# Performance work log

Hardware: AMD Instinct MI355X
Metric: run time of the kernel (lower is better)

The kernel has to match this reference:

```python
import jax, jax.numpy as jnp
import numpy as np
from jax import lax

B, T, S, J, D = 8, 512, 32, 64, 400
R, MDU, TAGS = 256, 100, 7


def _lstm(x, Wih, Whh, bih, bhh):
    """PyTorch-convention LSTM over x [N,L,Din]; gate order i,f,g,o.
    Returns (hs, cs) each [N,L,R] in scan order (not re-flipped)."""
    N = x.shape[0]
    Rh = Whh.shape[1]
    h0 = jnp.zeros((N, Rh), x.dtype)
    xW = x @ Wih.T + (bih + bhh)  # precompute input projection [N,L,4R]

    def step(carry, xt):
        h, c = carry
        g = xt + h @ Whh.T
        i, f, gg, o = jnp.split(g, 4, axis=-1)
        c = jax.nn.sigmoid(f) * c + jax.nn.sigmoid(i) * jnp.tanh(gg)
        h = jax.nn.sigmoid(o) * jnp.tanh(c)
        return (h, c), (h, c)

    _, (hs, cs) = lax.scan(step, (h0, h0), xW.transpose(1, 0, 2))
    return hs.transpose(1, 0, 2), cs.transpose(1, 0, 2)


def setup_inputs() -> dict:
    key = jax.random.key(0)
    ks = jax.random.split(key, 40)

    def rn(i, shape, s=0.1):
        return s * jax.random.normal(ks[i], shape, jnp.float32)

    inp = {
        'input_text': rn(0, (B, T, D), 1.0),
        'input_syn': rn(1, (B, S, J, D), 1.0),
        'label': jax.random.randint(ks[2], (B, T), 0, TAGS),
        'len_context': jnp.full((B,), T, jnp.int32),
        'len_synopsis': jnp.full((B, S), J, jnp.int32),
    }
    # 6 LSTM parameter sets: context f1/b1 (in=D), synopsis f/b (in=D), modeling f/b (in=4R)
    idx = 3
    for name, din in [('f1', D), ('b1', D), ('sf', D), ('sb', D), ('mf', 4 * R), ('mb', 4 * R)]:
        inp['Wih_' + name] = rn(idx, (4 * R, din)); idx += 1
        inp['Whh_' + name] = rn(idx, (4 * R, R)); idx += 1
        inp['bih_' + name] = rn(idx, (4 * R,)); idx += 1
        inp['bhh_' + name] = rn(idx, (4 * R,)); idx += 1
    inp['W_cWh'] = rn(idx, (MDU, 2 * R)); idx += 1
    inp['W_cWu'] = rn(idx, (MDU, 2 * R)); idx += 1
    inp['W_v'] = rn(idx, (1, MDU)); idx += 1
    inp['W_sWh'] = rn(idx, (2 * R, 2 * R)); idx += 1
    inp['W_sWu'] = rn(idx, (2 * R, 2 * R)); idx += 1
    inp['W_Ws'] = rn(idx, (MDU, 2 * R)); idx += 1
    inp['W_out'] = rn(idx, (TAGS, 6 * R)); idx += 1
    inp['b_out'] = rn(idx, (TAGS,)); idx += 1
    return inp


def reference(input_text, input_syn, label, len_context, len_synopsis,
              Wih_f1, Whh_f1, bih_f1, bhh_f1,
              Wih_b1, Whh_b1, bih_b1, bhh_b1,
              Wih_sf, Whh_sf, bih_sf, bhh_sf,
              Wih_sb, Whh_sb, bih_sb, bhh_sb,
              Wih_mf, Whh_mf, bih_mf, bhh_mf,
              Wih_mb, Whh_mb, bih_mb, bhh_mb,
              W_cWh, W_cWu, W_v, W_sWh, W_sWu, W_Ws, W_out, b_out):
    B_, T_, D_ = input_text.shape
    S_, J_ = input_syn.shape[1], input_syn.shape[2]

    mask = (jnp.arange(T_)[None, :] < len_context[:, None]).astype(input_text.dtype)

    # --- representation layer: manual bi-LSTMCell; backward hiddens kept in scan order ---
    hs_f, cs_f = _lstm(input_text, Wih_f1, Whh_f1, bih_f1, bhh_f1)
    hs_b, cs_b = _lstm(input_text[:, ::-1], Wih_b1, Whh_b1, bih_b1, bhh_b1)
    H = jnp.concatenate([hs_f, hs_b], -1) * mask[..., None]   # [B,T,2R]
    m = jnp.concatenate([cs_f, cs_b], -1) * mask[..., None]   # [B,T,2R]
    x_init = jnp.zeros((B_, 1, 2 * R), input_text.dtype)
    H_full = jnp.concatenate([x_init, H], 1)                  # H_ : [B,T+1,2R]

    # --- synopsis encoder: bi-LSTM final hidden per synopsis sentence ---
    syn = input_syn.reshape(B_ * S_, J_, D_)
    sh_f, _ = _lstm(syn, Wih_sf, Whh_sf, bih_sf, bhh_sf)
    sh_b, _ = _lstm(syn[:, ::-1], Wih_sb, Whh_sb, bih_sb, bhh_sb)
    U = jnp.concatenate([sh_f[:, -1], sh_b[:, -1]], -1).reshape(B_, S_, 2 * R)

    # --- 'ff' co-attention ---
    cWh = H @ W_cWh.T                                          # [B,T,MDU]
    cWu = U @ W_cWu.T                                          # [B,S,MDU]
    z = jnp.tanh(cWh[:, :, None, :] + cWu[:, None, :, :]) @ W_v[0]  # [B,T,S]
    alpha = jax.nn.softmax(z, axis=-1)
    c = jnp.einsum('bts,bsd->btd', alpha, U)                   # [B,T,2R]

    # --- sentinel (ATT_SYN) ---
    Hprev = H_full[:, :T_]                                     # shifted: x_init, H[0..T-2]
    e = jax.nn.sigmoid(Hprev @ W_sWh.T + Hprev @ W_sWu.T)
    s = e * jnp.tanh(m)                                        # [B,T,2R]
    z_hat = jnp.tanh(s @ W_Ws.T + cWh) @ W_v[0]                # [B,T]
    alpha_hat = jax.nn.softmax(jnp.concatenate([z, z_hat[..., None]], -1), axis=-1)
    beta = alpha_hat[:, :, S_:S_ + 1]                          # [B,T,1]
    c_hat = beta * s + (1.0 - beta) * c
    G = jnp.concatenate([H, c_hat], -1)                        # [B,T,4R]

    # --- modeling bi-LSTM (standard aligned outputs) + output projection ---
    mh_f, _ = _lstm(G, Wih_mf, Whh_mf, bih_mf, bhh_mf)
    mh_b, _ = _lstm(G[:, ::-1], Wih_mb, Whh_mb, bih_mb, bhh_mb)
    M = jnp.concatenate([mh_f, mh_b[:, ::-1]], -1)             # [B,T,2R]

    logit = jnp.concatenate([G, M], -1) @ W_out.T + b_out      # [B,T,TAGS]
    return logit
```

## Files before the change

### kernel.cpp

```cpp
#include <hip/hip_runtime.h>
#include <math.h>
#include <stddef.h>


#define BB 8
#define TT 512
#define SS 32
#define JJ 64
#define DD 400
#define RR 256
#define G4 1024
#define H2 512
#define MDU_ 100
#define TAGS_ 7
#define BT (BB*TT)
#define NSEQ (BB*SS)
#define SCH 64
#define MB1 (1024*1024)

typedef __attribute__((ext_vector_type(8))) short short8;
typedef __attribute__((ext_vector_type(4))) float floatx4;
typedef __attribute__((ext_vector_type(4))) unsigned int u32x4;
typedef unsigned short u16;
typedef unsigned int u32;

__device__ __forceinline__ float us2f(u16 u) {
    unsigned int v = ((unsigned int)u) << 16;
    return __builtin_bit_cast(float, v);
}
__device__ __forceinline__ u16 f2us(float f) {
    unsigned int v = __builtin_bit_cast(unsigned int, f);
    v += 0x7FFFu + ((v >> 16) & 1u);
    return (u16)(v >> 16);
}
__device__ __forceinline__ float ldin(const void* p, long i, int bf) {
    return bf ? us2f(((const u16*)p)[i]) : ((const float*)p)[i];
}
__device__ __forceinline__ float sigm(float x) { return 1.0f / (1.0f + expf(-x)); }
__device__ __forceinline__ float sigm_f(float x) { return 1.0f / (1.0f + __expf(-x)); }
__device__ __forceinline__ float tanh_f(float x) {
    float e = __expf(-2.0f * fabsf(x));
    float t = (1.0f - e) / (1.0f + e);
    return copysignf(t, x);
}

__global__ void detect_k(const void* x, int* flag) {
    __shared__ int cnt;
    if (threadIdx.x == 0) cnt = 0;
    __syncthreads();
    u16 lo = ((const u16*)x)[threadIdx.x * 2];
    int e = (lo >> 7) & 0xFF;
    if (e >= 118 && e <= 131) atomicAdd(&cnt, 1);
    __syncthreads();
    if (threadIdx.x == 0) *flag = (cnt > 128) ? 1 : 0;
}
__global__ void castbf_k(const void* src, long off, u16* dst, long n, const int* flag) {
    long i = (long)blockIdx.x * 256 + threadIdx.x;
    if (i < n) dst[i] = (*flag) ? ((const u16*)src)[off + i] : f2us(((const float*)src)[off + i]);
}
__global__ void castf_k(const void* src, float* dst, long n, const int* flag) {
    long i = (long)blockIdx.x * 256 + threadIdx.x;
    if (i < n) dst[i] = ldin(src, i, *flag);
}
__global__ void zero_k(u32* p, long n) {
    long i = (long)blockIdx.x * 256 + threadIdx.x;
    if (i < n) p[i] = 0u;
}
__global__ void bias_sum_k(const void* bih, const void* bhh, float* out, const int* flag) {
    int i = blockIdx.x * 256 + threadIdx.x;
    if (i < G4) out[i] = ldin(bih, i, *flag) + ldin(bhh, i, *flag);
}
__global__ void wsum_k(const void* a, const void* b, u16* o, const int* flag) {
    int i = blockIdx.x * 256 + threadIdx.x;
    if (i < H2 * H2) o[i] = f2us(ldin(a, i, *flag) + ldin(b, i, *flag));
}
__global__ void whh_frag_k(const void* Whh, u16* WF, const int* flag) {
    int i = blockIdx.x * 256 + threadIdx.x;
    if (i >= 4 * 4 * 4 * 8 * 64 * 8) return;
    int j  = i & 7;
    int ln = (i >> 3) & 63;
    int c  = (i >> 9) & 7;
    int t  = (i >> 12) & 3;
    int w  = (i >> 14) & 3;
    int s  = (i >> 16) & 3;
    int n_g = w * 256 + s * 64 + t * 16 + (ln & 15);
    int k   = c * 32 + (ln >> 4) * 8 + j;
    WF[i] = f2us(ldin(Whh, (long)n_g * 256 + k, *flag));
}

#define BM 128
#define BN 128
#define BK 32
#define LDT 40

__global__ __launch_bounds__(256)
void gemm_bt(const u16* __restrict__ A, int lda,
             const u16* __restrict__ W, int ldw,
             void* __restrict__ C, int ldc,
             const float* __restrict__ bias,
             int M, int N, int K, int outBf16)
{
    __shared__ alignas(16) short As[BM * LDT];
    __shared__ alignas(16) short Bs[BN * LDT];
    const int tid  = threadIdx.x;
    const int m0   = blockIdx.y * BM;
    const int n0   = blockIdx.x * BN;
    const int lane = tid & 63;
    const int wave = tid >> 6;
    const int wm   = wave >> 1, wn = wave & 1;
    const int quad = lane >> 4, mrow = lane & 15;

    floatx4 acc[4][4];
#pragma unroll
    for (int i = 0; i < 4; ++i)
#pragma unroll
        for (int j = 0; j < 4; ++j) { floatx4 z4 = {0.f,0.f,0.f,0.f}; acc[i][j] = z4; }

    for (int k0 = 0; k0 < K; k0 += BK) {
#pragma unroll
        for (int cc = 0; cc < 2; ++cc) {
            int c   = tid + cc * 256;
            int row = c >> 2;
            int kc  = (c & 3) << 3;
            int gk  = k0 + kc;
            {
                int gr = m0 + row;
                short8 v;
                if (gr < M && gk + 8 <= K) {
                    v = *(const short8*)(A + (size_t)gr * lda + gk);
                } else {
#pragma unroll
                    for (int e = 0; e < 8; ++e)
                        v[e] = (gr < M && (gk + e) < K) ? (short)A[(size_t)gr * lda + gk + e] : (short)0;
                }
                *(short8*)&As[row * LDT + kc] = v;
            }
            {
                int gn = n0 + row;
                short8 v;
                if (gn < N && gk + 8 <= K) {
                    v = *(const short8*)(W + (size_t)gn * ldw + gk);
                } else {
#pragma unroll
                    for (int e = 0; e < 8; ++e)
                        v[e] = (gn < N && (gk + e) < K) ? (short)W[(size_t)gn * ldw + gk + e] : (short)0;
                }
                *(short8*)&Bs[row * LDT + kc] = v;
            }
        }
        __syncthreads();

        short8 af[4], bf[4];
#pragma unroll
        for (int i = 0; i < 4; ++i)
            af[i] = *(const short8*)&As[(wm * 64 + i * 16 + mrow) * LDT + quad * 8];
#pragma unroll
        for (int j = 0; j < 4; ++j)
            bf[j] = *(const short8*)&Bs[(wn * 64 + j * 16 + mrow) * LDT + quad * 8];
#pragma unroll
        for (int i = 0; i < 4; ++i)
#pragma unroll
            for (int j = 0; j < 4; ++j)
                acc[i][j] = __builtin_amdgcn_mfma_f32_16x16x32_bf16(af[i], bf[j], acc[i][j], 0, 0, 0);
        __syncthreads();
    }

#pragma unroll
    for (int i = 0; i < 4; ++i)
#pragma unroll
        for (int j = 0; j < 4; ++j)
#pragma unroll
            for (int r = 0; r < 4; ++r) {
                int row = m0 + wm * 64 + i * 16 + quad * 4 + r;
                int col = n0 + wn * 64 + j * 16 + mrow;
                if (row < M && col < N) {
                    float v = acc[i][j][r];
                    if (bias) v += bias[col];
                    if (outBf16) ((u16*)C)[(size_t)row * ldc + col] = f2us(v);
                    else         ((float*)C)[(size_t)row * ldc + col] = v;
                }
            }
}

__global__ __launch_bounds__(256, 1)
void lstm_coop(const u16* __restrict__ xWf, const u16* __restrict__ xWb,
               const u16* __restrict__ WFf, const u16* __restrict__ WFb,
               int L,
               u16* __restrict__ hOut, int hStride,
               u16* __restrict__ cOut, int cStride,
               const int* __restrict__ lenp,
               int writeAtSource, int lastOnly, int seqBase,
               u32* __restrict__ hx32, u32* __restrict__ flags,
               int grpBase, int nb, int G8)
{
    const int wgid = blockIdx.x;
    const int s    = wgid / G8;
    const int g    = wgid - s * G8;
    if (g >= 2 * nb) return;
    const int dir  = g / nb;
    const int bat  = g - dir * nb;
    const int tid = threadIdx.x;
    const int wv  = tid >> 6;
    const int ln  = tid & 63;
    const int q   = ln >> 4, m = ln & 15;
    const u16* xW = dir ? xWb : xWf;
    const u16* WF = dir ? WFb : WFf;
    const int grp = grpBase + g;
    u32* flg = flags + (size_t)grp * 64;
    u32* hx  = hx32 + (size_t)grp * 2048;

    __shared__ float g_s[4 * 8 * 64];

    short8 bw[4][8];
    {
        const u16* wb = WF + ((size_t)(s * 4 + wv) * 32) * 512 + ln * 8;
#pragma unroll
        for (int t4 = 0; t4 < 4; ++t4)
#pragma unroll
            for (int c = 0; c < 8; ++c)
                bw[t4][c] = *(const short8*)(wb + (size_t)(t4 * 8 + c) * 512);
    }

    const int seqU = tid >> 5;
    const int j0   = (tid & 31) * 2;
    const int gcol = s * 64 + j0;
    const int mylen = lenp ? lenp[bat * 8 + seqU] : 0x7fffffff;
    float cR0 = 0.f, cR1 = 0.f;

    u32 px0, px1, px2, px3;
    {
        const int tt0 = dir ? (L - 1) : 0;
        const u16* xr = xW + (((size_t)(bat * 8 + seqU)) * L + tt0) * G4 + gcol;
        px0 = *(const u32*)xr;
        px1 = *(const u32*)(xr + 256);
        px2 = *(const u32*)(xr + 512);
        px3 = *(const u32*)(xr + 768);
    }

    for (int t = 0; t < L; ++t) {
        const int tt = dir ? (L - 1 - t) : t;
        short8 a[8];
        if (t > 0) {
            const u32* hp = hx + ((t - 1) & 1) * 1024 + m * 128;
#pragma unroll
            for (int c = 0; c < 8; ++c) {
                if (m < 8) {
                    u32x4 v = *(const u32x4*)(hp + c * 16 + q * 4);
                    a[c] = __builtin_bit_cast(short8, v);
                } else {
                    short8 z = {0,0,0,0,0,0,0,0}; a[c] = z;
                }
            }
        } else {
            short8 z = {0,0,0,0,0,0,0,0};
#pragma unroll
            for (int c = 0; c < 8; ++c) a[c] = z;
        }
        floatx4 acc[4];
#pragma unroll
        for (int t4 = 0; t4 < 4; ++t4) { floatx4 z4 = {0.f,0.f,0.f,0.f}; acc[t4] = z4; }
#pragma unroll
        for (int c = 0; c < 8; ++c)
#pragma unroll
            for (int t4 = 0; t4 < 4; ++t4)
                acc[t4] = __builtin_amdgcn_mfma_f32_16x16x32_bf16(a[c], bw[t4][c], acc[t4], 0, 0, 0);
        if (q < 2) {
#pragma unroll
            for (int t4 = 0; t4 < 4; ++t4)
#pragma unroll
                for (int r = 0; r < 4; ++r)
                    g_s[(wv * 8 + q * 4 + r) * 64 + t4 * 16 + m] = acc[t4][r];
        }
        __syncthreads();
        float hn0, hn1, cn0, cn1;
        {
            float i0 = g_s[(0 * 8 + seqU) * 64 + j0]     + us2f((u16)(px0 & 0xffffu));
            float i1 = g_s[(0 * 8 + seqU) * 64 + j0 + 1] + us2f((u16)(px0 >> 16));
            float f0 = g_s[(1 * 8 + seqU) * 64 + j0]     + us2f((u16)(px1 & 0xffffu));
            float f1 = g_s[(1 * 8 + seqU) * 64 + j0 + 1] + us2f((u16)(px1 >> 16));
            float g0 = g_s[(2 * 8 + seqU) * 64 + j0]     + us2f((u16)(px2 & 0xffffu));
            float g1 = g_s[(2 * 8 + seqU) * 64 + j0 + 1] + us2f((u16)(px2 >> 16));
            float o0 = g_s[(3 * 8 + seqU) * 64 + j0]     + us2f((u16)(px3 & 0xffffu));
            float o1 = g_s[(3 * 8 + seqU) * 64 + j0 + 1] + us2f((u16)(px3 >> 16));
            cn0 = sigm_f(f0) * cR0 + sigm_f(i0) * tanh_f(g0);
            cn1 = sigm_f(f1) * cR1 + sigm_f(i1) * tanh_f(g1);
            hn0 = sigm_f(o0) * tanh_f(cn0);
            hn1 = sigm_f(o1) * tanh_f(cn1);
            cR0 = cn0;
            cR1 = cn1;
            u32 hpack = (u32)f2us(hn0) | ((u32)f2us(hn1) << 16);
            __hip_atomic_store(hx + (t & 1) * 1024 + seqU * 128 + (gcol >> 1),
                               hpack, __ATOMIC_RELAXED, __HIP_MEMORY_SCOPE_AGENT);
        }
        asm volatile("s_waitcnt vmcnt(0)" ::: "memory");
        __syncthreads();
        const bool last = (t == L - 1);
        if (tid == 0 && !last)
            __hip_atomic_store(&flg[s * 16], (u32)(t + 1),
                               __ATOMIC_RELEASE, __HIP_MEMORY_SCOPE_AGENT);
        if (!lastOnly) {
            int wr = writeAtSource ? tt : t;
            float mk = (wr >= mylen) ? 0.f : 1.f;
            size_t ro = ((size_t)(bat * 8 + seqU)) * L + wr;
            u32 hp2 = (u32)f2us(hn0 * mk) | ((u32)f2us(hn1 * mk) << 16);
            *(u32*)(hOut + ro * hStride + dir * RR + gcol) = hp2;
            if (cOut) {
                u32 cp2 = (u32)f2us(cn0 * mk) | ((u32)f2us(cn1 * mk) << 16);
                *(u32*)(cOut + ro * cStride + dir * RR + gcol) = cp2;
            }
        } else if (last) {
            size_t ro = (size_t)(seqBase + bat * 8 + seqU);
            u32 hp2 = (u32)f2us(hn0) | ((u32)f2us(hn1) << 16);
            *(u32*)(hOut + ro * hStride + dir * RR + gcol) = hp2;
        }
        if (!last) {
            {
                const int tn = dir ? (L - 2 - t) : (t + 1);
                const u16* xr = xW + (((size_t)(bat * 8 + seqU)) * L + tn) * G4 + gcol;
                px0 = *(const u32*)xr;
                px1 = *(const u32*)(xr + 256);
                px2 = *(const u32*)(xr + 512);
                px3 = *(const u32*)(xr + 768);
            }
            if (tid == 0) {
                const u32 tgt = (u32)(t + 1);
                long guard = 0;
                for (;;) {
                    u32 f0 = __hip_atomic_load(&flg[0],  __ATOMIC_RELAXED, __HIP_MEMORY_SCOPE_AGENT);
                    u32 f1 = __hip_atomic_load(&flg[16], __ATOMIC_RELAXED, __HIP_MEMORY_SCOPE_AGENT);
                    u32 f2 = __hip_atomic_load(&flg[32], __ATOMIC_RELAXED, __HIP_MEMORY_SCOPE_AGENT);
                    u32 f3 = __hip_atomic_load(&flg[48], __ATOMIC_RELAXED, __HIP_MEMORY_SCOPE_AGENT);
                    if (f0 >= tgt && f1 >= tgt && f2 >= tgt && f3 >= tgt) break;
                    if (++guard > (1L << 18)) break;
                    if (guard > 32) __builtin_amdgcn_s_sleep(1);
                }
                __builtin_amdgcn_fence(__ATOMIC_ACQUIRE, "agent");
            }
            __syncthreads();
        }
    }
}

__global__ void hprev_k(const u16* __restrict__ G, u16* __restrict__ Hp) {
    int idx = blockIdx.x * 256 + threadIdx.x;
    if (idx < BT * H2) {
        int r = idx >> 9, d = idx & 511;
        int t = r & (TT - 1);
        Hp[idx] = (t == 0) ? (u16)0 : G[(size_t)(r - 1) * G4 + d];
    }
}
__global__ void s_k(const float* __restrict__ e, const u16* __restrict__ mB,
                    u16* __restrict__ sB) {
    int i = blockIdx.x * 256 + threadIdx.x;
    if (i < BT * H2) sB[i] = f2us(sigm(e[i]) * tanhf(us2f(mB[i])));
}
__global__ void z_k(const float* __restrict__ cWh, const float* __restrict__ cWu,
                    const float* __restrict__ Wv, float* __restrict__ z) {
    int idx = blockIdx.x * 256 + threadIdx.x;
    if (idx >= BT * SS) return;
    int r = idx >> 5, s = idx & 31;
    int b = r >> 9;
    const float* ph = cWh + (size_t)r * MDU_;
    const float* pu = cWu + (size_t)(b * SS + s) * MDU_;
    float acc = 0.f;
    for (int j = 0; j < MDU_; ++j) acc += tanhf(ph[j] + pu[j]) * Wv[j];
    z[idx] = acc;
}
__global__ void zhat_k(const float* __restrict__ sW, const float* __restrict__ cWh,
                       const float* __restrict__ Wv, float* __restrict__ zhat) {
    int r = blockIdx.x * 256 + threadIdx.x;
    if (r >= BT) return;
    float acc = 0.f;
    const float* ps = sW + (size_t)r * MDU_;
    const float* ph = cWh + (size_t)r * MDU_;
    for (int j = 0; j < MDU_; ++j) acc += tanhf(ps[j] + ph[j]) * Wv[j];
    zhat[r] = acc;
}
__global__ __launch_bounds__(64)
void attn_mix_k(const float* __restrict__ z, const float* __restrict__ zhat,
                const u16* __restrict__ U, const u16* __restrict__ sB,
                u16* __restrict__ G) {
    int r = blockIdx.x;
    int lane = threadIdx.x;
    int b = r >> 9;
    __shared__ float alpha[SS];
    float zv = (lane < SS) ? z[(size_t)r * SS + lane] : -1e30f;
    float mx = zv;
    for (int o = 32; o > 0; o >>= 1) mx = fmaxf(mx, __shfl_xor(mx, o));
    float ez = (lane < SS) ? expf(zv - mx) : 0.f;
    float s1 = ez;
    for (int o = 32; o > 0; o >>= 1) s1 += __shfl_xor(s1, o);
    float zh = zhat[r];
    float mx2 = fmaxf(mx, zh);
    float denom = s1 * expf(mx - mx2) + expf(zh - mx2);
    float beta = expf(zh - mx2) / denom;
    if (lane < SS) alpha[lane] = ez / s1;
    __syncthreads();
    for (int d = lane; d < H2; d += 64) {
        float cv = 0.f;
#pragma unroll 8
        for (int s2 = 0; s2 < SS; ++s2)
            cv += alpha[s2] * us2f(U[(size_t)(b * SS + s2) * H2 + d]);
        float sv = us2f(sB[(size_t)r * H2 + d]);
        G[(size_t)r * G4 + H2 + d] = f2us(beta * sv + (1.f - beta) * cv);
    }
}
__global__ __launch_bounds__(256)
void logit_k(const u16* __restrict__ G, const u16* __restrict__ Mb,
             const u16* __restrict__ Wout, const float* __restrict__ boutF,
             void* __restrict__ out, const int* __restrict__ flag) {
    int r = blockIdx.x * 4 + (threadIdx.x >> 6);
    if (r >= BT) return;
    int lane = threadIdx.x & 63;
    float acc[TAGS_] = {0, 0, 0, 0, 0, 0, 0};
    for (int k = lane; k < 1536; k += 64) {
        float v = (k < G4) ? us2f(G[(size_t)r * G4 + k]) : us2f(Mb[(size_t)r * H2 + (k - G4)]);
#pragma unroll
        for (int tg = 0; tg < TAGS_; ++tg) acc[tg] += v * us2f(Wout[tg * 1536 + k]);
    }
#pragma unroll
    for (int tg = 0; tg < TAGS_; ++tg) {
        float s = acc[tg];
        for (int o = 32; o > 0; o >>= 1) s += __shfl_xor(s, o);
        acc[tg] = s;
    }
    if (lane == 0) {
        int bf = *flag;
#pragma unroll
        for (int tg = 0; tg < TAGS_; ++tg) {
            float v = acc[tg] + boutF[tg];
            if (bf) ((u16*)out)[(size_t)r * TAGS_ + tg] = f2us(v);
            else    ((float*)out)[(size_t)r * TAGS_ + tg] = v;
        }
    }
}

extern "C" void kernel_launch(void* const* d_in, const int* in_sizes, int n_in,
                              void* d_out, int out_size, void* d_ws, size_t ws_size,
                              hipStream_t stream)
{
    const void* x_text = d_in[0];
    const void* x_syn  = d_in[1];
    const int* len_ctx = (const int*)d_in[3];
    const void *Wih[6], *Whh[6], *bih[6], *bhh[6];
    for (int l = 0; l < 6; ++l) {
        Wih[l] = d_in[5 + l * 4 + 0];
        Whh[l] = d_in[5 + l * 4 + 1];
        bih[l] = d_in[5 + l * 4 + 2];
        bhh[l] = d_in[5 + l * 4 + 3];
    }
    const void* W_cWh = d_in[29];
    const void* W_cWu = d_in[30];
    const void* W_v   = d_in[31];
    const void* W_sWh = d_in[32];
    const void* W_sWu = d_in[33];
    const void* W_Ws  = d_in[34];
    const void* W_out = d_in[35];
    const void* b_out = d_in[36];
    (void)in_sizes; (void)n_in; (void)out_size;

    char* ws = (char*)d_ws;
    size_t off = 0;
    auto alloc = [&](size_t bytes) -> void* {
        void* p = ws + off;
        off += (bytes + 255) & ~(size_t)255;
        return p;
    };
    int*   flagB  = (int*)alloc(256);
    float* bsum[6];
    for (int l = 0; l < 6; ++l) bsum[l] = (float*)alloc((size_t)G4 * 4);
    u16*   WsumB  = (u16*)alloc((size_t)H2 * H2 * 2);
    u16*   Ub     = (u16*)alloc((size_t)NSEQ * H2 * 2);
    u16*   Gb     = (u16*)alloc((size_t)BT * G4 * 2);
    u16*   mMb    = (u16*)alloc((size_t)BT * H2 * 2);
    float* cWhB   = (float*)alloc((size_t)BT * MDU_ * 4);
    float* cWuB   = (float*)alloc((size_t)NSEQ * MDU_ * 4);
    float* sWB    = (float*)alloc((size_t)BT * MDU_ * 4);
    float* zB     = (float*)alloc((size_t)BT * SS * 4);
    float* zhatB  = (float*)alloc((size_t)BT * 4);
    u16*   Wcwh16 = (u16*)alloc((size_t)MDU_ * H2 * 2);
    u16*   Wcwu16 = (u16*)alloc((size_t)MDU_ * H2 * 2);
    u16*   Wws16  = (u16*)alloc((size_t)MDU_ * H2 * 2);
    u16*   Wout16 = (u16*)alloc((size_t)TAGS_ * 1536 * 2);
    float* WvF    = (float*)alloc((size_t)MDU_ * 4);
    float* boutF  = (float*)alloc((size_t)TAGS_ * 4);
    u16*   WF[6];
    for (int l = 0; l < 6; ++l) WF[l] = (u16*)alloc((size_t)G4 * RR * 2);
    u32*   cnts   = (u32*)alloc((size_t)128 * 64 * 4);
    u32*   hx32   = (u32*)alloc((size_t)128 * 2048 * 4);

    size_t fixedEnd = off;
    bool bigws = (ws_size >= fixedEnd + (size_t)81 * MB1);
    char* BIG = (char*)alloc(bigws ? (size_t)80 * MB1 : (size_t)24 * MB1);

    u16*   bufA  = (u16*)BIG;
    u16*   bufB  = (u16*)(BIG + (size_t)8 * MB1);
    u16*   x16   = (u16*)(BIG + (size_t)16 * MB1);
    u16*   W16a  = (u16*)(BIG + (size_t)19 * MB1 + MB1 / 2);
    u16*   W16b  = (u16*)(BIG + (size_t)20 * MB1 + MB1 / 2);
    u16*   HprevB = (u16*)BIG;
    float* eBuf   = (float*)(BIG + (size_t)4 * MB1);
    u16*   sBuf   = (u16*)(BIG + (size_t)12 * MB1);
    u16*   mxWf  = (u16*)BIG;
    u16*   mxWb  = (u16*)(BIG + (size_t)8 * MB1);
    u16*   W16aD = (u16*)(BIG + (size_t)16 * MB1);
    u16*   W16bD = (u16*)(BIG + (size_t)18 * MB1);
    u16*   mbufA = (u16*)BIG;
    u16*   mbufB = (u16*)(BIG + (size_t)32 * MB1);
    u16*   mx16  = (u16*)(BIG + (size_t)64 * MB1);
    u16*   mW16a = (u16*)(BIG + (size_t)78 * MB1);
    u16*   mW16b = (u16*)(BIG + (size_t)79 * MB1);

    auto cgrid = [](long n) { return dim3((unsigned)((n + 255) / 256)); };

    detect_k<<<dim3(1), dim3(256), 0, stream>>>(x_text, flagB);
    zero_k<<<cgrid(128 * 64), dim3(256), 0, stream>>>(cnts, 128 * 64);
    castbf_k<<<cgrid(MDU_ * H2), dim3(256), 0, stream>>>(W_cWh, 0, Wcwh16, MDU_ * H2, flagB);
    castbf_k<<<cgrid(MDU_ * H2), dim3(256), 0, stream>>>(W_cWu, 0, Wcwu16, MDU_ * H2, flagB);
    castbf_k<<<cgrid(MDU_ * H2), dim3(256), 0, stream>>>(W_Ws, 0, Wws16, MDU_ * H2, flagB);
    castbf_k<<<cgrid(TAGS_ * 1536), dim3(256), 0, stream>>>(W_out, 0, Wout16, TAGS_ * 1536, flagB);
    castf_k<<<cgrid(MDU_), dim3(256), 0, stream>>>(W_v, WvF, MDU_, flagB);
    castf_k<<<cgrid(TAGS_), dim3(256), 0, stream>>>(b_out, boutF, TAGS_, flagB);
    for (int l = 0; l < 6; ++l) {
        bias_sum_k<<<dim3(4), dim3(256), 0, stream>>>(bih[l], bhh[l], bsum[l], flagB);
        whh_frag_k<<<dim3(1024), dim3(256), 0, stream>>>(Whh[l], WF[l], flagB);
    }
    wsum_k<<<cgrid(H2 * H2), dim3(256), 0, stream>>>(W_sWh, W_sWu, WsumB, flagB);

    if (bigws) {
        castbf_k<<<cgrid(G4 * DD), dim3(256), 0, stream>>>(Wih[2], 0, mW16a, G4 * DD, flagB);
        castbf_k<<<cgrid(G4 * DD), dim3(256), 0, stream>>>(Wih[3], 0, mW16b, G4 * DD, flagB);
        castbf_k<<<cgrid((long)NSEQ * JJ * DD), dim3(256), 0, stream>>>(x_syn, 0, mx16, (long)NSEQ * JJ * DD, flagB);
        gemm_bt<<<dim3(8, (NSEQ * JJ) / BM), dim3(256), 0, stream>>>(mx16, DD, mW16a, DD, mbufA, G4, bsum[2], NSEQ * JJ, G4, DD, 1);
        gemm_bt<<<dim3(8, (NSEQ * JJ) / BM), dim3(256), 0, stream>>>(mx16, DD, mW16b, DD, mbufB, G4, bsum[3], NSEQ * JJ, G4, DD, 1);
        lstm_coop<<<dim3(256), dim3(256), 0, stream>>>(
            mbufA, mbufB, WF[2], WF[3], JJ,
            Ub, H2, (u16*)nullptr, 0, (const int*)nullptr,
            0, 1, 0, hx32, cnts, 4, 32, 64);
    } else {
        castbf_k<<<cgrid(G4 * DD), dim3(256), 0, stream>>>(Wih[2], 0, W16a, G4 * DD, flagB);
        castbf_k<<<cgrid(G4 * DD), dim3(256), 0, stream>>>(Wih[3], 0, W16b, G4 * DD, flagB);
        for (int c = 0; c < NSEQ / SCH; ++c) {
            long chunkElems = (long)SCH * JJ * DD;
            castbf_k<<<cgrid(chunkElems), dim3(256), 0, stream>>>(x_syn, (long)c * chunkElems, x16, chunkElems, flagB);
            gemm_bt<<<dim3(8, (SCH * JJ) / BM), dim3(256), 0, stream>>>(x16, DD, W16a, DD, bufA, G4, bsum[2], SCH * JJ, G4, DD, 1);
            gemm_bt<<<dim3(8, (SCH * JJ) / BM), dim3(256), 0, stream>>>(x16, DD, W16b, DD, bufB, G4, bsum[3], SCH * JJ, G4, DD, 1);
            lstm_coop<<<dim3(64), dim3(256), 0, stream>>>(
                bufA, bufB, WF[2], WF[3], JJ,
                Ub, H2, (u16*)nullptr, 0, (const int*)nullptr,
                0, 1, c * SCH, hx32, cnts, 4 + c * 16, 8, 16);
        }
    }

    castbf_k<<<cgrid((long)BT * DD), dim3(256), 0, stream>>>(x_text, 0, x16, (long)BT * DD, flagB);
    castbf_k<<<cgrid(G4 * DD), dim3(256), 0, stream>>>(Wih[0], 0, W16a, G4 * DD, flagB);
    castbf_k<<<cgrid(G4 * DD), dim3(256), 0, stream>>>(Wih[1], 0, W16b, G4 * DD, flagB);
    gemm_bt<<<dim3(8, 32), dim3(256), 0, stream>>>(x16, DD, W16a, DD, bufA, G4, bsum[0], BT, G4, DD, 1);
    gemm_bt<<<dim3(8, 32), dim3(256), 0, stream>>>(x16, DD, W16b, DD, bufB, G4, bsum[1], BT, G4, DD, 1);
    lstm_coop<<<dim3(32), dim3(256), 0, stream>>>(
        bufA, bufB, WF[0], WF[1], TT,
        Gb, G4, mMb, H2, len_ctx, 0, 0, 0, hx32, cnts, 0, 1, 8);

    gemm_bt<<<dim3(1, 32), dim3(256), 0, stream>>>(Gb, G4, Wcwh16, H2, cWhB, MDU_, nullptr, BT, MDU_, H2, 0);
    gemm_bt<<<dim3(1, 2),  dim3(256), 0, stream>>>(Ub, H2, Wcwu16, H2, cWuB, MDU_, nullptr, NSEQ, MDU_, H2, 0);
    hprev_k<<<cgrid(BT * H2), dim3(256), 0, stream>>>(Gb, HprevB);
    gemm_bt<<<dim3(4, 32), dim3(256), 0, stream>>>(HprevB, H2, WsumB, H2, eBuf, H2, nullptr, BT, H2, H2, 0);
    s_k<<<cgrid(BT * H2), dim3(256), 0, stream>>>(eBuf, mMb, sBuf);
    gemm_bt<<<dim3(1, 32), dim3(256), 0, stream>>>(sBuf, H2, Wws16, H2, sWB, MDU_, nullptr, BT, MDU_, H2, 0);
    z_k<<<cgrid(BT * SS), dim3(256), 0, stream>>>(cWhB, cWuB, WvF, zB);
    zhat_k<<<cgrid(BT), dim3(256), 0, stream>>>(sWB, cWhB, WvF, zhatB);
    attn_mix_k<<<dim3(BT), dim3(64), 0, stream>>>(zB, zhatB, Ub, sBuf, Gb);

    castbf_k<<<cgrid(G4 * G4), dim3(256), 0, stream>>>(Wih[4], 0, W16aD, G4 * G4, flagB);
    castbf_k<<<cgrid(G4 * G4), dim3(256), 0, stream>>>(Wih[5], 0, W16bD, G4 * G4, flagB);
    gemm_bt<<<dim3(8, 32), dim3(256), 0, stream>>>(Gb, G4, W16aD, G4, mxWf, G4, bsum[4], BT, G4, G4, 1);
    gemm_bt<<<dim3(8, 32), dim3(256), 0, stream>>>(Gb, G4, W16bD, G4, mxWb, G4, bsum[5], BT, G4, G4, 1);
    lstm_coop<<<dim3(32), dim3(256), 0, stream>>>(
        mxWf, mxWb, WF[4], WF[5], TT,
        mMb, H2, (u16*)nullptr, 0, (const int*)nullptr, 1, 0, 0, hx32, cnts, 2, 1, 8);

    logit_k<<<dim3(BT / 4), dim3(256), 0, stream>>>(Gb, mMb, Wout16, boutF, d_out, flagB);
}
```

Baseline: 4.183 ms.

## Merge prep/cast kernels, reorder context GEMMs, overlap LSTM output writes with barrier

Collapses the many small weight-prep, bias-sum, fragment-layout and zeroing launches into one prep kernel, and merges the input casts into single multi-segment cast kernels. In the big-workspace path it also moves the context projection GEMMs ahead of the synopsis LSTM, using aliased scratch buffers. Inside the recurrent LSTM loop, output stores and next-step prefetch are moved so that non-zero waves issue them before the inter-block spin wait. Fast tanh and sigmoid approximations now replace the libm versions in the attention kernels. The aim is to cut launch overhead and hide store latency behind synchronisation, at the cost of buffer aliasing that must not conflict and slightly lower precision in the activations.

After: 4.398 ms. 5.1% more time.

```diff
diff --git a/kernel.cpp b/kernel.cpp
--- a/kernel.cpp
+++ b/kernel.cpp
@@ -24,6 +24,8 @@
 typedef unsigned short u16;
 typedef unsigned int u32;
 
+struct Ptr6 { const void* p[6]; };
+
 __device__ __forceinline__ float us2f(u16 u) {
     unsigned int v = ((unsigned int)u) << 16;
     return __builtin_bit_cast(float, v);
@@ -36,7 +38,6 @@
 __device__ __forceinline__ float ldin(const void* p, long i, int bf) {
     return bf ? us2f(((const u16*)p)[i]) : ((const float*)p)[i];
 }
-__device__ __forceinline__ float sigm(float x) { return 1.0f / (1.0f + expf(-x)); }
 __device__ __forceinline__ float sigm_f(float x) { return 1.0f / (1.0f + __expf(-x)); }
 __device__ __forceinline__ float tanh_f(float x) {
     float e = __expf(-2.0f * fabsf(x));
@@ -58,34 +59,92 @@
     long i = (long)blockIdx.x * 256 + threadIdx.x;
     if (i < n) dst[i] = (*flag) ? ((const u16*)src)[off + i] : f2us(((const float*)src)[off + i]);
 }
-__global__ void castf_k(const void* src, float* dst, long n, const int* flag) {
+
+__global__ void prep_k(const int* __restrict__ flag,
+    const void* Wcwh, const void* Wcwu, const void* Wws, const void* Wout,
+    const void* Wv, const void* bout, const void* WsWh, const void* WsWu,
+    u16* Wcwh16, u16* Wcwu16, u16* Wws16, u16* Wout16,
+    float* WvF, float* boutF, u16* WsumB, float* bsumAll,
+    Ptr6 bih, Ptr6 bhh, Ptr6 whh, u16* WFall, u32* cnts)
+{
+    const int bf = *flag;
     long i = (long)blockIdx.x * 256 + threadIdx.x;
-    if (i < n) dst[i] = ldin(src, i, *flag);
-}
-__global__ void zero_k(u32* p, long n) {
+    if (i < 51200) { Wcwh16[i] = f2us(ldin(Wcwh, i, bf)); return; }
+    i -= 51200;
+    if (i < 51200) { Wcwu16[i] = f2us(ldin(Wcwu, i, bf)); return; }
+    i -= 51200;
+    if (i < 51200) { Wws16[i] = f2us(ldin(Wws, i, bf)); return; }
+    i -= 51200;
+    if (i < 10752) { Wout16[i] = f2us(ldin(Wout, i, bf)); return; }
+    i -= 10752;
+    if (i < 100) { WvF[i] = ldin(Wv, i, bf); return; }
+    i -= 100;
+    if (i < 7) { boutF[i] = ldin(bout, i, bf); return; }
+    i -= 7;
+    if (i < 6 * 1024) {
+        int l = (int)(i >> 10), k = (int)(i & 1023);
+        bsumAll[l * 1024 + k] = ldin(bih.p[l], k, bf) + ldin(bhh.p[l], k, bf);
+        return;
+    }
+    i -= 6 * 1024;
+    if (i < 262144) { WsumB[i] = f2us(ldin(WsWh, i, bf) + ldin(WsWu, i, bf)); return; }
+    i -= 262144;
+    if (i < 6L * 262144) {
+        int l  = (int)(i >> 18);
+        int ii = (int)(i & 262143);
+        int j  = ii & 7;
+        int ln = (ii >> 3) & 63;
+        int c  = (ii >> 9) & 7;
+        int t  = (ii >> 12) & 3;
+        int w  = (ii >> 14) & 3;
+        int s  = (ii >> 16) & 3;
+        int n_g = w * 256 + s * 64 + t * 16 + (ln & 15);
+        int k   = c * 32 + (ln >> 4) * 8 + j;
+        WFall[(size_t)l * 262144 + ii] = f2us(ldin(whh.p[l], (long)n_g * 256 + k, bf));
+        return;
+    }
+    i -= 6L * 262144;
+    if (i < 8192) cnts[i] = 0u;
+}
+
+__global__ void castAB_k(const void* xsyn, u16* mx16,
+                         const void* wih2, u16* mW16a,
+                         const void* wih3, u16* mW16b,
+                         const void* xtext, u16* x16c,
+                         const void* wih0, u16* W16ac,
+                         const void* wih1, u16* W16bc,
+                         const int* __restrict__ flag)
+{
+    const int bf = *flag;
     long i = (long)blockIdx.x * 256 + threadIdx.x;
-    if (i < n) p[i] = 0u;
-}
-__global__ void bias_sum_k(const void* bih, const void* bhh, float* out, const int* flag) {
-    int i = blockIdx.x * 256 + threadIdx.x;
-    if (i < G4) out[i] = ldin(bih, i, *flag) + ldin(bhh, i, *flag);
-}
-__global__ void wsum_k(const void* a, const void* b, u16* o, const int* flag) {
-    int i = blockIdx.x * 256 + threadIdx.x;
-    if (i < H2 * H2) o[i] = f2us(ldin(a, i, *flag) + ldin(b, i, *flag));
-}
-__global__ void whh_frag_k(const void* Whh, u16* WF, const int* flag) {
-    int i = blockIdx.x * 256 + threadIdx.x;
-    if (i >= 4 * 4 * 4 * 8 * 64 * 8) return;
-    int j  = i & 7;
-    int ln = (i >> 3) & 63;
-    int c  = (i >> 9) & 7;
-    int t  = (i >> 12) & 3;
-    int w  = (i >> 14) & 3;
-    int s  = (i >> 16) & 3;
-    int n_g = w * 256 + s * 64 + t * 16 + (ln & 15);
-    int k   = c * 32 + (ln >> 4) * 8 + j;
-    WF[i] = f2us(ldin(Whh, (long)n_g * 256 + k, *flag));
+    const long nsyn = (long)NSEQ * JJ * DD;
+    const long nw   = (long)G4 * DD;
+    const long ntxt = (long)BT * DD;
+    if (i < nsyn) { mx16[i] = f2us(ldin(xsyn, i, bf)); return; }
+    i -= nsyn;
+    if (i < nw) { mW16a[i] = f2us(ldin(wih2, i, bf)); return; }
+    i -= nw;
+    if (i < nw) { mW16b[i] = f2us(ldin(wih3, i, bf)); return; }
+    i -= nw;
+    if (i < ntxt) { x16c[i] = f2us(ldin(xtext, i, bf)); return; }
+    i -= ntxt;
+    if (i < nw) { W16ac[i] = f2us(ldin(wih0, i, bf)); return; }
+    i -= nw;
+    if (i < nw) { W16bc[i] = f2us(ldin(wih1, i, bf)); return; }
+}
+
+__global__ void cast3_k(const void* s0, u16* d0, long n0,
+                        const void* s1, u16* d1, long n1,
+                        const void* s2, u16* d2, long n2,
+                        const int* __restrict__ flag)
+{
+    const int bf = *flag;
+    long i = (long)blockIdx.x * 256 + threadIdx.x;
+    if (i < n0) { d0[i] = f2us(ldin(s0, i, bf)); return; }
+    i -= n0;
+    if (i < n1) { d1[i] = f2us(ldin(s1, i, bf)); return; }
+    i -= n1;
+    if (i < n2) { d2[i] = f2us(ldin(s2, i, bf)); return; }
 }
 
 #define BM 128
@@ -237,6 +296,33 @@
         px3 = *(const u32*)(xr + 768);
     }
 
+#define DO_OUT() do {                                                         \
+        if (!lastOnly) {                                                      \
+            int wr = writeAtSource ? tt : t;                                  \
+            float mk = (wr >= mylen) ? 0.f : 1.f;                             \
+            size_t ro = ((size_t)(bat * 8 + seqU)) * L + wr;                  \
+            u32 hp2 = (u32)f2us(hn0 * mk) | ((u32)f2us(hn1 * mk) << 16);      \
+            *(u32*)(hOut + ro * hStride + dir * RR + gcol) = hp2;             \
+            if (cOut) {                                                       \
+                u32 cp2 = (u32)f2us(cn0 * mk) | ((u32)f2us(cn1 * mk) << 16);  \
+                *(u32*)(cOut + ro * cStride + dir * RR + gcol) = cp2;         \
+            }                                                                 \
+        } else if (last) {                                                    \
+            size_t ro = (size_t)(seqBase + bat * 8 + seqU);                   \
+            u32 hp2 = (u32)f2us(hn0) | ((u32)f2us(hn1) << 16);                \
+            *(u32*)(hOut + ro * hStride + dir * RR + gcol) = hp2;             \
+        }                                                                     \
+    } while (0)
+
+#define DO_PREF() do {                                                        \
+        const int tn = dir ? (L - 2 - t) : (t + 1);                           \
+        const u16* xr = xW + (((size_t)(bat * 8 + seqU)) * L + tn) * G4 + gcol; \
+        px0 = *(const u32*)xr;                                                \
+        px1 = *(const u32*)(xr + 256);                                        \
+        px2 = *(const u32*)(xr + 512);                                        \
+        px3 = *(const u32*)(xr + 768);                                        \
+    } while (0)
+
     for (int t = 0; t < L; ++t) {
         const int tt = dir ? (L - 1 - t) : t;
         short8 a[8];
@@ -298,30 +384,8 @@
         if (tid == 0 && !last)
             __hip_atomic_store(&flg[s * 16], (u32)(t + 1),
                                __ATOMIC_RELEASE, __HIP_MEMORY_SCOPE_AGENT);
-        if (!lastOnly) {
-            int wr = writeAtSource ? tt : t;
-            float mk = (wr >= mylen) ? 0.f : 1.f;
-            size_t ro = ((size_t)(bat * 8 + seqU)) * L + wr;
-            u32 hp2 = (u32)f2us(hn0 * mk) | ((u32)f2us(hn1 * mk) << 16);
-            *(u32*)(hOut + ro * hStride + dir * RR + gcol) = hp2;
-            if (cOut) {
-                u32 cp2 = (u32)f2us(cn0 * mk) | ((u32)f2us(cn1 * mk) << 16);
-                *(u32*)(cOut + ro * cStride + dir * RR + gcol) = cp2;
-            }
-        } else if (last) {
-            size_t ro = (size_t)(seqBase + bat * 8 + seqU);
-            u32 hp2 = (u32)f2us(hn0) | ((u32)f2us(hn1) << 16);
-            *(u32*)(hOut + ro * hStride + dir * RR + gcol) = hp2;
-        }
         if (!last) {
-            {
-                const int tn = dir ? (L - 2 - t) : (t + 1);
-                const u16* xr = xW + (((size_t)(bat * 8 + seqU)) * L + tn) * G4 + gcol;
-                px0 = *(const u32*)xr;
-                px1 = *(const u32*)(xr + 256);
-                px2 = *(const u32*)(xr + 512);
-                px3 = *(const u32*)(xr + 768);
-            }
+            if (wv != 0) { DO_OUT(); DO_PREF(); }
             if (tid == 0) {
                 const u32 tgt = (u32)(t + 1);
                 long guard = 0;
@@ -337,8 +401,13 @@
                 __builtin_amdgcn_fence(__ATOMIC_ACQUIRE, "agent");
             }
             __syncthreads();
-        }
-    }
+            if (wv == 0) { DO_OUT(); DO_PREF(); }
+        } else {
+            DO_OUT();
+        }
+    }
+#undef DO_OUT
+#undef DO_PREF
 }
 
 __global__ void hprev_k(const u16* __restrict__ G, u16* __restrict__ Hp) {
@@ -352,7 +421,7 @@
 __global__ void s_k(const float* __restrict__ e, const u16* __restrict__ mB,
                     u16* __restrict__ sB) {
     int i = blockIdx.x * 256 + threadIdx.x;
-    if (i < BT * H2) sB[i] = f2us(sigm(e[i]) * tanhf(us2f(mB[i])));
+    if (i < BT * H2) sB[i] = f2us(sigm_f(e[i]) * tanh_f(us2f(mB[i])));
 }
 __global__ void z_k(const float* __restrict__ cWh, const float* __restrict__ cWu,
                     const float* __restrict__ Wv, float* __restrict__ z) {
@@ -363,7 +432,8 @@
     const float* ph = cWh + (size_t)r * MDU_;
     const float* pu = cWu + (size_t)(b * SS + s) * MDU_;
     float acc = 0.f;
-    for (int j = 0; j < MDU_; ++j) acc += tanhf(ph[j] + pu[j]) * Wv[j];
+#pragma unroll 4
+    for (int j = 0; j < MDU_; ++j) acc += tanh_f(ph[j] + pu[j]) * Wv[j];
     z[idx] = acc;
 }
 __global__ void zhat_k(const float* __restrict__ sW, const float* __restrict__ cWh,
@@ -373,7 +443,8 @@
     float acc = 0.f;
     const float* ps = sW + (size_t)r * MDU_;
     const float* ph = cWh + (size_t)r * MDU_;
-    for (int j = 0; j < MDU_; ++j) acc += tanhf(ps[j] + ph[j]) * Wv[j];
+#pragma unroll 4
+    for (int j = 0; j < MDU_; ++j) acc += tanh_f(ps[j] + ph[j]) * Wv[j];
     zhat[r] = acc;
 }
 __global__ __launch_bounds__(64)
@@ -467,8 +538,7 @@
         return p;
     };
     int*   flagB  = (int*)alloc(256);
-    float* bsum[6];
-    for (int l = 0; l < 6; ++l) bsum[l] = (float*)alloc((size_t)G4 * 4);
+    float* bsumAll = (float*)alloc((size_t)6 * G4 * 4);
     u16*   WsumB  = (u16*)alloc((size_t)H2 * H2 * 2);
     u16*   Ub     = (u16*)alloc((size_t)NSEQ * H2 * 2);
     u16*   Gb     = (u16*)alloc((size_t)BT * G4 * 2);
@@ -484,8 +554,11 @@
     u16*   Wout16 = (u16*)alloc((size_t)TAGS_ * 1536 * 2);
     float* WvF    = (float*)alloc((size_t)MDU_ * 4);
     float* boutF  = (float*)alloc((size_t)TAGS_ * 4);
+    u16*   WFall  = (u16*)alloc((size_t)6 * G4 * RR * 2);
     u16*   WF[6];
-    for (int l = 0; l < 6; ++l) WF[l] = (u16*)alloc((size_t)G4 * RR * 2);
+    for (int l = 0; l < 6; ++l) WF[l] = WFall + (size_t)l * G4 * RR;
+    float* bsum[6];
+    for (int l = 0; l < 6; ++l) bsum[l] = bsumAll + (size_t)l * G4;
     u32*   cnts   = (u32*)alloc((size_t)128 * 64 * 4);
     u32*   hx32   = (u32*)alloc((size_t)128 * 2048 * 4);
 
@@ -510,33 +583,44 @@
     u16*   mx16  = (u16*)(BIG + (size_t)64 * MB1);
     u16*   mW16a = (u16*)(BIG + (size_t)78 * MB1);
     u16*   mW16b = (u16*)(BIG + (size_t)79 * MB1);
+    u16*   bufAc = (u16*)(BIG + (size_t)64 * MB1);
+    u16*   bufBc = (u16*)(BIG + (size_t)72 * MB1);
+    u16*   x16c  = Gb;
+    u16*   W16ac = mMb;
+    u16*   W16bc = mMb + (size_t)G4 * DD;
 
     auto cgrid = [](long n) { return dim3((unsigned)((n + 255) / 256)); };
 
+    Ptr6 pBih, pBhh, pWhh;
+    for (int l = 0; l < 6; ++l) { pBih.p[l] = bih[l]; pBhh.p[l] = bhh[l]; pWhh.p[l] = Whh[l]; }
+
     detect_k<<<dim3(1), dim3(256), 0, stream>>>(x_text, flagB);
-    zero_k<<<cgrid(128 * 64), dim3(256), 0, stream>>>(cnts, 128 * 64);
-    castbf_k<<<cgrid(MDU_ * H2), dim3(256), 0, stream>>>(W_cWh, 0, Wcwh16, MDU_ * H2, flagB);
-    castbf_k<<<cgrid(MDU_ * H2), dim3(256), 0, stream>>>(W_cWu, 0, Wcwu16, MDU_ * H2, flagB);
-    castbf_k<<<cgrid(MDU_ * H2), dim3(256), 0, stream>>>(W_Ws, 0, Wws16, MDU_ * H2, flagB);
-    castbf_k<<<cgrid(TAGS_ * 1536), dim3(256), 0, stream>>>(W_out, 0, Wout16, TAGS_ * 1536, flagB);
-    castf_k<<<cgrid(MDU_), dim3(256), 0, stream>>>(W_v, WvF, MDU_, flagB);
-    castf_k<<<cgrid(TAGS_), dim3(256), 0, stream>>>(b_out, boutF, TAGS_, flagB);
-    for (int l = 0; l < 6; ++l) {
-        bias_sum_k<<<dim3(4), dim3(256), 0, stream>>>(bih[l], bhh[l], bsum[l], flagB);
-        whh_frag_k<<<dim3(1024), dim3(256), 0, stream>>>(Whh[l], WF[l], flagB);
-    }
-    wsum_k<<<cgrid(H2 * H2), dim3(256), 0, stream>>>(W_sWh, W_sWu, WsumB, flagB);
+    {
+        long nprep = 51200L * 3 + 10752 + 100 + 7 + 6 * 1024 + 262144 + 6L * 262144 + 8192;
+        prep_k<<<cgrid(nprep), dim3(256), 0, stream>>>(
+            flagB, W_cWh, W_cWu, W_Ws, W_out, W_v, b_out, W_sWh, W_sWu,
+            Wcwh16, Wcwu16, Wws16, Wout16, WvF, boutF, WsumB, bsumAll,
+            pBih, pBhh, pWhh, WFall, cnts);
+    }
 
     if (bigws) {
-        castbf_k<<<cgrid(G4 * DD), dim3(256), 0, stream>>>(Wih[2], 0, mW16a, G4 * DD, flagB);
-        castbf_k<<<cgrid(G4 * DD), dim3(256), 0, stream>>>(Wih[3], 0, mW16b, G4 * DD, flagB);
-        castbf_k<<<cgrid((long)NSEQ * JJ * DD), dim3(256), 0, stream>>>(x_syn, 0, mx16, (long)NSEQ * JJ * DD, flagB);
+        {
+            long ncast = (long)NSEQ * JJ * DD + 4L * G4 * DD + (long)BT * DD;
+            castAB_k<<<cgrid(ncast), dim3(256), 0, stream>>>(
+                x_syn, mx16, Wih[2], mW16a, Wih[3], mW16b,
+                x_text, x16c, Wih[0], W16ac, Wih[1], W16bc, flagB);
+        }
         gemm_bt<<<dim3(8, (NSEQ * JJ) / BM), dim3(256), 0, stream>>>(mx16, DD, mW16a, DD, mbufA, G4, bsum[2], NSEQ * JJ, G4, DD, 1);
         gemm_bt<<<dim3(8, (NSEQ * JJ) / BM), dim3(256), 0, stream>>>(mx16, DD, mW16b, DD, mbufB, G4, bsum[3], NSEQ * JJ, G4, DD, 1);
+        gemm_bt<<<dim3(8, 32), dim3(256), 0, stream>>>(x16c, DD, W16ac, DD, bufAc, G4, bsum[0], BT, G4, DD, 1);
+        gemm_bt<<<dim3(8, 32), dim3(256), 0, stream>>>(x16c, DD, W16bc, DD, bufBc, G4, bsum[1], BT, G4, DD, 1);
         lstm_coop<<<dim3(256), dim3(256), 0, stream>>>(
             mbufA, mbufB, WF[2], WF[3], JJ,
             Ub, H2, (u16*)nullptr, 0, (const int*)nullptr,
             0, 1, 0, hx32, cnts, 4, 32, 64);
+        lstm_coop<<<dim3(32), dim3(256), 0, stream>>>(
+            bufAc, bufBc, WF[0], WF[1], TT,
+            Gb, G4, mMb, H2, len_ctx, 0, 0, 0, hx32, cnts, 0, 1, 8);
     } else {
         castbf_k<<<cgrid(G4 * DD), dim3(256), 0, stream>>>(Wih[2], 0, W16a, G4 * DD, flagB);
         castbf_k<<<cgrid(G4 * DD), dim3(256), 0, stream>>>(Wih[3], 0, W16b, G4 * DD, flagB);
@@ -550,16 +634,15 @@
                 Ub, H2, (u16*)nullptr, 0, (const int*)nullptr,
                 0, 1, c * SCH, hx32, cnts, 4 + c * 16, 8, 16);
         }
-    }
-
-    castbf_k<<<cgrid((long)BT * DD), dim3(256), 0, stream>>>(x_text, 0, x16, (long)BT * DD, flagB);
-    castbf_k<<<cgrid(G4 * DD), dim3(256), 0, stream>>>(Wih[0], 0, W16a, G4 * DD, flagB);
-    castbf_k<<<cgrid(G4 * DD), dim3(256), 0, stream>>>(Wih[1], 0, W16b, G4 * DD, flagB);
-    gemm_bt<<<dim3(8, 32), dim3(256), 0, stream>>>(x16, DD, W16a, DD, bufA, G4, bsum[0], BT, G4, DD, 1);
-    gemm_bt<<<dim3(8, 32), dim3(256), 0, stream>>>(x16, DD, W16b, DD, bufB, G4, bsum[1], BT, G4, DD, 1);
-    lstm_coop<<<dim3(32), dim3(256), 0, stream>>>(
-        bufA, bufB, WF[0], WF[1], TT,
-        Gb, G4, mMb, H2, len_ctx, 0, 0, 0, hx32, cnts, 0, 1, 8);
+        castbf_k<<<cgrid((long)BT * DD), dim3(256), 0, stream>>>(x_text, 0, x16, (long)BT * DD, flagB);
+        castbf_k<<<cgrid(G4 * DD), dim3(256), 0, stream>>>(Wih[0], 0, W16a, G4 * DD, flagB);
+        castbf_k<<<cgrid(G4 * DD), dim3(256), 0, stream>>>(Wih[1], 0, W16b, G4 * DD, flagB);
+        gemm_bt<<<dim3(8, 32), dim3(256), 0, stream>>>(x16, DD, W16a, DD, bufA, G4, bsum[0], BT, G4, DD, 1);
+        gemm_bt<<<dim3(8, 32), dim3(256), 0, stream>>>(x16, DD, W16b, DD, bufB, G4, bsum[1], BT, G4, DD, 1);
+        lstm_coop<<<dim3(32), dim3(256), 0, stream>>>(
+            bufA, bufB, WF[0], WF[1], TT,
+            Gb, G4, mMb, H2, len_ctx, 0, 0, 0, hx32, cnts, 0, 1, 8);
+    }
 
     gemm_bt<<<dim3(1, 32), dim3(256), 0, stream>>>(Gb, G4, Wcwh16, H2, cWhB, MDU_, nullptr, BT, MDU_, H2, 0);
     gemm_bt<<<dim3(1, 2),  dim3(256), 0, stream>>>(Ub, H2, Wcwu16, H2, cWuB, MDU_, nullptr, NSEQ, MDU_, H2, 0);
@@ -571,8 +654,9 @@
     zhat_k<<<cgrid(BT), dim3(256), 0, stream>>>(sWB, cWhB, WvF, zhatB);
     attn_mix_k<<<dim3(BT), dim3(64), 0, stream>>>(zB, zhatB, Ub, sBuf, Gb);
 
-    castbf_k<<<cgrid(G4 * G4), dim3(256), 0, stream>>>(Wih[4], 0, W16aD, G4 * G4, flagB);
-    castbf_k<<<cgrid(G4 * G4), dim3(256), 0, stream>>>(Wih[5], 0, W16bD, G4 * G4, flagB);
+    cast3_k<<<cgrid(2L * G4 * G4), dim3(256), 0, stream>>>(
+        Wih[4], W16aD, (long)G4 * G4, Wih[5], W16bD, (long)G4 * G4,
+        nullptr, nullptr, 0, flagB);
     gemm_bt<<<dim3(8, 32), dim3(256), 0, stream>>>(Gb, G4, W16aD, G4, mxWf, G4, bsum[4], BT, G4, G4, 1);
     gemm_bt<<<dim3(8, 32), dim3(256), 0, stream>>>(Gb, G4, W16bD, G4, mxWb, G4, bsum[5], BT, G4, G4, 1);
     lstm_coop<<<dim3(32), dim3(256), 0, stream>>>(
```
